# Optimization experiments

Hardware: AMD Instinct MI355X
Metric: run time of the kernel (lower is better)

## Reference

```python
import jax, jax.numpy as jnp
import numpy as np

D_MODEL = 1024
N_HEADS = 16
HEAD_DIM = D_MODEL // N_HEADS


def setup_inputs() -> dict:
    key = jax.random.key(0)
    ks = jax.random.split(key, 5)
    x = jax.random.normal(ks[0], (4, 2048, D_MODEL), dtype=jnp.float32)
    s = 1.0 / np.sqrt(D_MODEL)
    W_qkv = jax.random.normal(ks[1], (D_MODEL, 3 * D_MODEL), dtype=jnp.float32) * s
    b_qkv = jnp.zeros((3 * D_MODEL,), dtype=jnp.float32)
    W_proj = jax.random.normal(ks[2], (D_MODEL, D_MODEL), dtype=jnp.float32) * s
    b_proj = jnp.zeros((D_MODEL,), dtype=jnp.float32)
    return {"x": x, "W_qkv": W_qkv, "b_qkv": b_qkv, "W_proj": W_proj, "b_proj": b_proj}


def reference(x, W_qkv, b_qkv, W_proj, b_proj):
    B, T, C = x.shape
    H, Dh = N_HEADS, HEAD_DIM
    qkv = x @ W_qkv + b_qkv                      # [B,T,3C]
    q, k, v = jnp.split(qkv, 3, axis=-1)
    # [B,T,C] -> [B,H,T,Dh]
    q = q.reshape(B, T, H, Dh).transpose(0, 2, 1, 3)
    k = k.reshape(B, T, H, Dh).transpose(0, 2, 1, 3)
    v = v.reshape(B, T, H, Dh).transpose(0, 2, 1, 3)
    scale = 1.0 / np.sqrt(Dh)
    att = jnp.einsum("bhqd,bhkd->bhqk", q, k) * scale
    causal = jnp.tril(jnp.ones((T, T), dtype=bool))
    att = jnp.where(causal, att, -jnp.inf)
    att = jax.nn.softmax(att, axis=-1)
    y = jnp.einsum("bhqk,bhkd->bhqd", att, v)    # [B,H,T,Dh]
    y = y.transpose(0, 2, 1, 3).reshape(B, T, C)
    return y @ W_proj + b_proj
```

## Files before the change

### kernel.cpp

```cpp
#include <hip/hip_runtime.h>
#include <hip/hip_bf16.h>
#include <cstdint>
#include <math.h>

#define DM   1024
#define NH   16
#define DH   64
#define BB   4
#define TT   2048
#define MTOT (BB*TT)

using short8 = __attribute__((ext_vector_type(8))) short;
using f32x4  = __attribute__((ext_vector_type(4))) float;

__device__ __forceinline__ f32x4 mfma16(short8 a, short8 b, f32x4 c) {
  return __builtin_amdgcn_mfma_f32_16x16x32_bf16(a, b, c, 0, 0, 0);
}

typedef const __attribute__((address_space(1))) unsigned int* as1_u32p;
typedef __attribute__((address_space(3))) unsigned int*       as3_u32p;

__device__ __forceinline__ void gl_lds16(const void* g, void* l) {
  __builtin_amdgcn_global_load_lds(
      (as1_u32p)(reinterpret_cast<uintptr_t>(g)),
      (as3_u32p)((unsigned int)(reinterpret_cast<uintptr_t>(l))),
      16, 0, 0);
}

__device__ __forceinline__ int swz64(int row, int col) {
  return row*64 + ((((col >> 3) ^ (row & 7)) << 3) | (col & 7));
}

__device__ __forceinline__ unsigned pkbf(float a, float b) {
  __hip_bfloat162 h = __float22bfloat162_rn(make_float2(a, b));
  return *reinterpret_cast<unsigned*>(&h);
}

__device__ __forceinline__ void perm16p(unsigned &a, unsigned &b) {
  asm("v_permlane16_swap_b32 %0, %1" : "+v"(a), "+v"(b));
}
__device__ __forceinline__ void perm32p(unsigned &a, unsigned &b) {
  asm("v_permlane32_swap_b32 %0, %1" : "+v"(a), "+v"(b));
}

__device__ __forceinline__ short8 ldsr_o0(unsigned a) {
  short8 r; asm volatile("ds_read_b128 %0, %1" : "=v"(r) : "v"(a)); return r;
}
__device__ __forceinline__ short8 ldsr_o1(unsigned a) {
  short8 r; asm volatile("ds_read_b128 %0, %1 offset:2048" : "=v"(r) : "v"(a)); return r;
}
__device__ __forceinline__ short8 ldsr_o2(unsigned a) {
  short8 r; asm volatile("ds_read_b128 %0, %1 offset:4096" : "=v"(r) : "v"(a)); return r;
}
__device__ __forceinline__ short8 ldsr_o3(unsigned a) {
  short8 r; asm volatile("ds_read_b128 %0, %1 offset:6144" : "=v"(r) : "v"(a)); return r;
}

#define LGKM0  do { asm volatile("s_waitcnt lgkmcnt(0)"); __builtin_amdgcn_sched_barrier(0); } while(0)
#define VMCNT6 do { __builtin_amdgcn_sched_barrier(0); asm volatile("s_waitcnt vmcnt(6)"); __builtin_amdgcn_sched_barrier(0); } while(0)
#define VMCNT0 do { __builtin_amdgcn_sched_barrier(0); asm volatile("s_waitcnt vmcnt(0)"); __builtin_amdgcn_sched_barrier(0); } while(0)
#define BARRIER do { __builtin_amdgcn_s_barrier(); __builtin_amdgcn_sched_barrier(0); } while(0)

__global__ __launch_bounds__(256) void k_cvt(const float* __restrict__ in,
                                             __hip_bfloat16* __restrict__ out, int n8) {
  int i = blockIdx.x * 256 + threadIdx.x;
  if (i >= n8) return;
  const float* p = in + (size_t)i * 8;
  short8 o;
#pragma unroll
  for (int j = 0; j < 8; ++j) {
    __hip_bfloat16 h = __float2bfloat16(p[j]);
    o[j] = *reinterpret_cast<short*>(&h);
  }
  *reinterpret_cast<short8*>(out + (size_t)i * 8) = o;
}

__global__ __launch_bounds__(256) void k_transpose_cvt(const float* __restrict__ W,
                                                       __hip_bfloat16* __restrict__ Wt,
                                                       int K, int N) {
  __shared__ float tbuf[32][33];
  const int n0 = blockIdx.x * 32, k0 = blockIdx.y * 32;
  const int tx = threadIdx.x & 31, ty = threadIdx.x >> 5;
#pragma unroll
  for (int i = 0; i < 4; ++i)
    tbuf[ty + i*8][tx] = W[(size_t)(k0 + ty + i*8) * N + n0 + tx];
  __syncthreads();
#pragma unroll
  for (int i = 0; i < 4; ++i)
    Wt[(size_t)(n0 + ty + i*8) * K + k0 + tx] = __float2bfloat16(tbuf[tx][ty + i*8]);
}

template <int EPI>
__global__ __launch_bounds__(512, 2) void k_gemm2(const __hip_bfloat16* __restrict__ A,
                                                  const __hip_bfloat16* __restrict__ Bt,
                                                  const float* __restrict__ bias,
                                                  float* __restrict__ outF,
                                                  __hip_bfloat16* __restrict__ Qb,
                                                  __hip_bfloat16* __restrict__ Kb,
                                                  __hip_bfloat16* __restrict__ Vtb) {
  __shared__ __hip_bfloat16 As[3][256 * 64];
  __shared__ __hip_bfloat16 Bs[3][128 * 64];
  const int tid = threadIdx.x;
  const int l = tid & 63, w = tid >> 6;
  const int lr = l & 15, lg = l >> 4;
  const int wm = w >> 1, wn = w & 1;
  const int m0 = blockIdx.x * 256, n0 = blockIdx.y * 128;

  const int srow = tid >> 3;
  const int scol = (((tid & 7) ^ (srow & 7)) << 3);
  const size_t aoffs = (size_t)(m0 + srow) * 1024 + scol;
  const size_t boffs = (size_t)(n0 + srow) * 1024 + scol;
  const int ldst = tid * 8;

  auto stage = [&](int t, int s) {
    const int k0 = t * 64;
    __hip_bfloat16* as_ = &As[s][0];
    __hip_bfloat16* bs_ = &Bs[s][0];
#pragma unroll
    for (int rd = 0; rd < 4; ++rd)
      gl_lds16(A + aoffs + (size_t)rd * 65536 + k0, as_ + rd * 4096 + ldst);
#pragma unroll
    for (int rd = 0; rd < 2; ++rd)
      gl_lds16(Bt + boffs + (size_t)rd * 65536 + k0, bs_ + rd * 4096 + ldst);
  };

  const unsigned asLds = (unsigned)(uintptr_t)&As[0][0];
  const unsigned bsLds = (unsigned)(uintptr_t)&Bs[0][0];
  const unsigned aBase = asLds + 2u * ((wm*64 + lr) * 64 + ((lg ^ (lr & 7)) << 3));
  const unsigned bBase = bsLds + 2u * ((wn*64 + lr) * 64 + ((lg ^ (lr & 7)) << 3));

  stage(0, 0);
  stage(1, 1);
  VMCNT6;
  BARRIER;

  f32x4 acc[4][4] = {};
  short8 a_[4][2], b_[2][2];

#pragma unroll
  for (int t = 0; t < 16; ++t) {
    const int s = t % 3;
    const unsigned aB0 = aBase + (unsigned)s * 32768u;
    const unsigned aB1 = aB0 ^ 64u;
    const unsigned bB0 = bBase + (unsigned)s * 16384u;
    const unsigned bB1 = bB0 ^ 64u;
    if (t + 2 < 16) stage(t + 2, (t + 2) % 3);
    a_[0][0] = ldsr_o0(aB0); a_[1][0] = ldsr_o1(aB0); a_[2][0] = ldsr_o2(aB0); a_[3][0] = ldsr_o3(aB0);
    a_[0][1] = ldsr_o0(aB1); a_[1][1] = ldsr_o1(aB1); a_[2][1] = ldsr_o2(aB1); a_[3][1] = ldsr_o3(aB1);
    b_[0][0] = ldsr_o0(bB0); b_[1][0] = ldsr_o1(bB0);
    b_[0][1] = ldsr_o0(bB1); b_[1][1] = ldsr_o1(bB1);
    LGKM0;
    __builtin_amdgcn_s_setprio(1);
#pragma unroll
    for (int m = 0; m < 4; ++m)
#pragma unroll
      for (int n = 0; n < 2; ++n)
#pragma unroll
        for (int ks = 0; ks < 2; ++ks)
          acc[m][n] = mfma16(a_[m][ks], b_[n][ks], acc[m][n]);
    __builtin_amdgcn_s_setprio(0);
    b_[0][0] = ldsr_o2(bB0); b_[1][0] = ldsr_o3(bB0);
    b_[0][1] = ldsr_o2(bB1); b_[1][1] = ldsr_o3(bB1);
    LGKM0;
    __builtin_amdgcn_s_setprio(1);
#pragma unroll
    for (int m = 0; m < 4; ++m)
#pragma unroll
      for (int n = 0; n < 2; ++n)
#pragma unroll
        for (int ks = 0; ks < 2; ++ks)
          acc[m][n + 2] = mfma16(a_[m][ks], b_[n][ks], acc[m][n + 2]);
    __builtin_amdgcn_s_setprio(0);
    if (t <= 13) { VMCNT6; }
    else if (t == 14) { VMCNT0; }
    BARRIER;
  }

  __syncthreads();
  if (EPI == 0) {
    __hip_bfloat16* reg = &As[0][0] + w * 4096;
    const int colbase = n0 + wn * 64;
    const int which = colbase >> 10;
    const int hh = (colbase >> 6) & 15;
    const float qs = 0.18033688011112042f;
#pragma unroll
    for (int n = 0; n < 4; ++n) {
      const int lc = n * 16 + lr;
      const float bv = bias[colbase + lc];
#pragma unroll
      for (int m = 0; m < 4; ++m) {
#pragma unroll
        for (int r = 0; r < 4; ++r) {
          const int lrow = m * 16 + lg * 4 + r;
          float v = acc[m][n][r] + bv;
          if (which == 0) v *= qs;
          const __hip_bfloat16 hv = __float2bfloat16(v);
          if (which == 2) reg[swz64(lc, lrow)] = hv;
          else            reg[swz64(lrow, lc)] = hv;
        }
      }
    }
    const int rowbase = m0 + wm * 64;
    const int b = rowbase >> 11;
    const size_t bh = (size_t)b * 16 + hh;
    const int g = l >> 2, i = l & 3;
    if (which < 2) {
      __hip_bfloat16* base = (which == 0) ? Qb : Kb;
#pragma unroll
      for (int j = 0; j < 4; ++j) {
        const int lrow = j * 16 + g;
        const int t = (rowbase & 2047) + lrow;
        __hip_bfloat16* dst = base + (bh * TT + t) * 64 + i * 16;
        short8 y0 = *reinterpret_cast<const short8*>(&reg[swz64(lrow, i * 16)]);
        short8 y1 = *reinterpret_cast<const short8*>(&reg[swz64(lrow, i * 16 + 8)]);
        *reinterpret_cast<short8*>(dst) = y0;
        *reinterpret_cast<short8*>(dst + 8) = y1;
      }
    } else {
#pragma unroll
      for (int j = 0; j < 4; ++j) {
        const int dd = j * 16 + g;
        const int t = (rowbase & 2047) + i * 16;
        __hip_bfloat16* dst = Vtb + (bh * 64 + dd) * TT + t;
        short8 y0 = *reinterpret_cast<const short8*>(&reg[swz64(dd, i * 16)]);
        short8 y1 = *reinterpret_cast<const short8*>(&reg[swz64(dd, i * 16 + 8)]);
        *reinterpret_cast<short8*>(dst) = y0;
        *reinterpret_cast<short8*>(dst + 8) = y1;
      }
    }
  } else {
#pragma unroll
    for (int n = 0; n < 4; ++n) {
      const int col = n0 + wn * 64 + n * 16 + lr;
      const float bv = bias[col];
#pragma unroll
      for (int m = 0; m < 4; ++m)
#pragma unroll
        for (int r = 0; r < 4; ++r) {
          const int row = m0 + wm * 64 + m * 16 + lg * 4 + r;
          outF[(size_t)row * 1024 + col] = acc[m][n][r] + bv;
        }
    }
  }
}

__device__ __forceinline__ void tile_step(f32x4 s0, f32x4 s1, int kbase, int kmaxw, int qmb,
                                          short8 v0, short8 v1, short8 v2, short8 v3,
                                          f32x4 (&acc)[4], float& lrun) {
  if (kbase + 31 > kmaxw - 15) {
#pragma unroll
    for (int r = 0; r < 4; ++r) {
      const int off = (r & 1) + ((r & 2) << 2);
      if (kbase + off > qmb)      s0[r] = -INFINITY;
      if (kbase + 16 + off > qmb) s1[r] = -INFINITY;
    }
  }
  float p0 = __builtin_amdgcn_exp2f(s0[0]), p1 = __builtin_amdgcn_exp2f(s0[1]);
  float p2 = __builtin_amdgcn_exp2f(s0[2]), p3 = __builtin_amdgcn_exp2f(s0[3]);
  float p4 = __builtin_amdgcn_exp2f(s1[0]), p5 = __builtin_amdgcn_exp2f(s1[1]);
  float p6 = __builtin_amdgcn_exp2f(s1[2]), p7 = __builtin_amdgcn_exp2f(s1[3]);
  lrun += ((p0 + p1) + (p2 + p3)) + ((p4 + p5) + (p6 + p7));
  unsigned u0 = pkbf(p0, p1);
  unsigned u1 = pkbf(p2, p3);
  unsigned u2 = pkbf(p4, p5);
  unsigned u3 = pkbf(p6, p7);
  perm16p(u0, u1);
  perm16p(u2, u3);
  perm32p(u0, u2);
  perm32p(u1, u3);
  union { unsigned u[4]; short8 s; } pw;
  pw.u[0] = u0; pw.u[1] = u2; pw.u[2] = u1; pw.u[3] = u3;
  const short8 pf = pw.s;
  acc[0] = mfma16(v0, pf, acc[0]);
  acc[1] = mfma16(v1, pf, acc[1]);
  acc[2] = mfma16(v2, pf, acc[2]);
  acc[3] = mfma16(v3, pf, acc[3]);
}

__device__ __forceinline__ void store_tile(__hip_bfloat16* Ylds, f32x4 (&acc)[4],
                                           float lrun, int q0, int w, int l,
                                           int lr, int lg, int bh,
                                           __hip_bfloat16* __restrict__ Y) {
  lrun += __shfl_xor(lrun, 16);
  lrun += __shfl_xor(lrun, 32);
  const float inv = 1.f / lrun;
#pragma unroll
  for (int nb = 0; nb < 4; ++nb) {
#pragma unroll
    for (int r = 0; r < 4; ++r) {
      const int d = nb * 16 + lg * 4 + r;
      Ylds[swz64(lr, d)] = __float2bfloat16(acc[nb][r] * inv);
    }
  }
  const int rr = l >> 2, part = l & 3;
  const int trow = q0 + w * 16 + rr;
  const int b = bh >> 4, h = bh & 15;
  short8 y0 = *reinterpret_cast<const short8*>(&Ylds[swz64(rr, part * 16)]);
  short8 y1 = *reinterpret_cast<const short8*>(&Ylds[swz64(rr, part * 16 + 8)]);
  __hip_bfloat16* dst = Y + ((size_t)b * TT + trow) * 1024 + h * 64 + part * 16;
  *reinterpret_cast<short8*>(dst) = y0;
  *reinterpret_cast<short8*>(dst + 8) = y1;
}

__global__ __launch_bounds__(256, 4) void k_flash(const __hip_bfloat16* __restrict__ Qb,
                                                  const __hip_bfloat16* __restrict__ Kb,
                                                  const __hip_bfloat16* __restrict__ Vtb,
                                                  __hip_bfloat16* __restrict__ Y) {
  __shared__ __hip_bfloat16 Klds[128 * 64];
  __shared__ __hip_bfloat16 Vtlds[64 * 128];
  const int tid = threadIdx.x;
  const int l = tid & 63, w = tid >> 6;
  const int lr = l & 15, lg = l >> 4;
  const int p  = blockIdx.x >> 6;
  const int bh = blockIdx.x & 63;
  const int q0A = p * 64, q0B = (31 - p) * 64;
  const __hip_bfloat16* Qp = Qb + (size_t)bh * TT * 64;
  const __hip_bfloat16* Kp = Kb + (size_t)bh * TT * 64;
  const __hip_bfloat16* Vp = Vtb + (size_t)bh * 64 * TT;
  const int qrowA = q0A + w * 16 + lr;
  const int qrowB = q0B + w * 16 + lr;
  const short8 qfA0 = *reinterpret_cast<const short8*>(Qp + (size_t)qrowA * 64 + lg * 8);
  const short8 qfA1 = *reinterpret_cast<const short8*>(Qp + (size_t)qrowA * 64 + 32 + lg * 8);
  const short8 qfB0 = *reinterpret_cast<const short8*>(Qp + (size_t)qrowB * 64 + lg * 8);
  const short8 qfB1 = *reinterpret_cast<const short8*>(Qp + (size_t)qrowB * 64 + 32 + lg * 8);
  f32x4 accA[4] = {}, accB[4] = {};
  float lA = 0.f, lB = 0.f;

  const int ka  = lr * 64 + ((lg ^ (lr & 7)) << 3);
  const int va  = lr * 128 + ((lg ^ (lr & 15)) << 3);

  const __hip_bfloat16* gk[4];
  const __hip_bfloat16* gv[4];
  __hip_bfloat16* lk[4];
  __hip_bfloat16* lv[4];
#pragma unroll
  for (int it = 0; it < 4; ++it) {
    int e = it * 2048 + tid * 8;
    int rowk = e >> 6;
    int lcolk = ((((e >> 3) & 7) ^ (rowk & 7)) << 3);
    int rk = rowk & 15;
    int srk = (((rk >> 1) ^ (rk >> 3)) & 1) ? (rk ^ 10) : rk;
    int rowks = (rowk & ~15) | srk;
    gk[it] = Kp + (size_t)rowks * 64 + lcolk;
    lk[it] = &Klds[e];
    int rowv = e >> 7;
    int lcolv = ((((e >> 3) & 15) ^ (rowv & 15)) << 3);
    gv[it] = Vp + (size_t)rowv * TT + lcolv;
    lv[it] = &Vtlds[e];
  }

  const int kmaxwA = q0A + w * 16 + 15;
  const int kmaxwB = q0B + w * 16 + 15;
  const int base_lg = ((lg & 1) << 2) | (lg & 2);
  const int qmbA = qrowA - base_lg;
  const int qmbB = qrowB - base_lg;
  const int nblk = (q0B + 63) / 128 + 1;
  for (int blk = 0; blk < nblk; ++blk) {
    const int kv0 = blk * 128;
#pragma unroll
    for (int it = 0; it < 4; ++it) {
      gl_lds16(gk[it], lk[it]);
      gk[it] += 128 * 64;
    }
#pragma unroll
    for (int it = 0; it < 4; ++it) {
      gl_lds16(gv[it], lv[it]);
      gv[it] += 128;
    }
    __syncthreads();
#pragma unroll
    for (int kci = 0; kci < 4; ++kci) {
      const int kbase = kv0 + kci * 32;
      if (kbase > kmaxwB) break;
      const int kb = ka + kci * 2048;
      const short8 kf00 = *reinterpret_cast<const short8*>(&Klds[kb]);
      const short8 kf10 = *reinterpret_cast<const short8*>(&Klds[kb + 1024]);
      const short8 kf01 = *reinterpret_cast<const short8*>(&Klds[kb ^ 32]);
      const short8 kf11 = *reinterpret_cast<const short8*>(&Klds[(kb + 1024) ^ 32]);
      f32x4 sB0 = {}, sB1 = {};
      sB0 = mfma16(kf00, qfB0, sB0);
      sB1 = mfma16(kf10, qfB0, sB1);
      sB0 = mfma16(kf01, qfB1, sB0);
      sB1 = mfma16(kf11, qfB1, sB1);
      const bool aAct = (kbase <= kmaxwA);
      f32x4 sA0 = {}, sA1 = {};
      if (aAct) {
        sA0 = mfma16(kf00, qfA0, sA0);
        sA1 = mfma16(kf10, qfA0, sA1);
        sA0 = mfma16(kf01, qfA1, sA0);
        sA1 = mfma16(kf11, qfA1, sA1);
      }
      const int vb = va ^ (kci * 32);
      const short8 v0 = *reinterpret_cast<const short8*>(&Vtlds[vb]);
      const short8 v1 = *reinterpret_cast<const short8*>(&Vtlds[vb + 2048]);
      const short8 v2 = *reinterpret_cast<const short8*>(&Vtlds[vb + 4096]);
      const short8 v3 = *reinterpret_cast<const short8*>(&Vtlds[vb + 6144]);
      tile_step(sB0, sB1, kbase, kmaxwB, qmbB, v0, v1, v2, v3, accB, lB);
      if (aAct)
        tile_step(sA0, sA1, kbase, kmaxwA, qmbA, v0, v1, v2, v3, accA, lA);
    }
    __syncthreads();
  }
  __hip_bfloat16* Ylds = Klds + w * 1024;
  store_tile(Ylds, accA, lA, q0A, w, l, lr, lg, bh, Y);
  store_tile(Ylds, accB, lB, q0B, w, l, lr, lg, bh, Y);
}

extern "C" void kernel_launch(void* const* d_in, const int* in_sizes, int n_in,
                              void* d_out, int out_size, void* d_ws, size_t ws_size,
                              hipStream_t stream) {
  const float* x     = (const float*)d_in[0];
  const float* Wqkv  = (const float*)d_in[1];
  const float* bqkv  = (const float*)d_in[2];
  const float* Wproj = (const float*)d_in[3];
  const float* bproj = (const float*)d_in[4];

  char* ws = (char*)d_ws;
  size_t off = 0;
  auto alloc = [&](size_t bytes) {
    char* p = ws + off;
    off += (bytes + 255) & ~(size_t)255;
    return p;
  };
  __hip_bfloat16* xb    = (__hip_bfloat16*)alloc((size_t)MTOT * 1024 * 2);
  __hip_bfloat16* wqkvT = (__hip_bfloat16*)alloc((size_t)3072 * 1024 * 2);
  __hip_bfloat16* wpT   = (__hip_bfloat16*)alloc((size_t)1024 * 1024 * 2);
  __hip_bfloat16* Qb    = (__hip_bfloat16*)alloc((size_t)64 * TT * 64 * 2);
  __hip_bfloat16* Kb    = (__hip_bfloat16*)alloc((size_t)64 * TT * 64 * 2);
  __hip_bfloat16* Vtb   = (__hip_bfloat16*)alloc((size_t)64 * TT * 64 * 2);
  __hip_bfloat16* Yb    = (__hip_bfloat16*)alloc((size_t)MTOT * 1024 * 2);

  k_cvt<<<(MTOT * 1024 / 8 + 255) / 256, 256, 0, stream>>>(x, xb, MTOT * 1024 / 8);
  k_transpose_cvt<<<dim3(3072 / 32, 1024 / 32), 256, 0, stream>>>(Wqkv, wqkvT, 1024, 3072);
  k_transpose_cvt<<<dim3(1024 / 32, 1024 / 32), 256, 0, stream>>>(Wproj, wpT, 1024, 1024);
  k_gemm2<0><<<dim3(32, 24), 512, 0, stream>>>(xb, wqkvT, bqkv, nullptr, Qb, Kb, Vtb);
  k_flash<<<16 * 64, 256, 0, stream>>>(Qb, Kb, Vtb, Yb);
  k_gemm2<1><<<dim3(32, 8), 512, 0, stream>>>(Yb, wpT, bproj, (float*)d_out,
                                              nullptr, nullptr, nullptr);
}
```

Baseline: 152.3 us.

## Add dedicated QKV GEMM kernel with 256x192 tiles and double buffering

Adds a separate QKV projection kernel that uses 256x192 output tiles instead of 256x128, with a 2-stage LDS pipeline in place of 3 stages. Each wave accumulates a 64x96 sub-tile in two MFMA phases. The grid drops from 32x24 to 32x16 blocks, so each block reuses its A tile across more columns. The epilogue is rewritten to scatter Q/K/V per 16-column group through LDS. The risks are higher register pressure from 24 accumulators per wave, shallower prefetch with a full vmcnt(0) wait every iteration, and possible tail effects from the new block count.

```diff
diff --git a/kernel.cpp b/kernel.cpp
--- a/kernel.cpp
+++ b/kernel.cpp
@@ -55,6 +55,12 @@
 __device__ __forceinline__ short8 ldsr_o3(unsigned a) {
   short8 r; asm volatile("ds_read_b128 %0, %1 offset:6144" : "=v"(r) : "v"(a)); return r;
 }
+__device__ __forceinline__ short8 ldsr_o4(unsigned a) {
+  short8 r; asm volatile("ds_read_b128 %0, %1 offset:8192" : "=v"(r) : "v"(a)); return r;
+}
+__device__ __forceinline__ short8 ldsr_o5(unsigned a) {
+  short8 r; asm volatile("ds_read_b128 %0, %1 offset:10240" : "=v"(r) : "v"(a)); return r;
+}
 
 #define LGKM0  do { asm volatile("s_waitcnt lgkmcnt(0)"); __builtin_amdgcn_sched_barrier(0); } while(0)
 #define VMCNT6 do { __builtin_amdgcn_sched_barrier(0); asm volatile("s_waitcnt vmcnt(6)"); __builtin_amdgcn_sched_barrier(0); } while(0)
@@ -90,14 +96,156 @@
     Wt[(size_t)(n0 + ty + i*8) * K + k0 + tx] = __float2bfloat16(tbuf[tx][ty + i*8]);
 }
 
-template <int EPI>
+__global__ __launch_bounds__(512, 2) void k_gemm3(const __hip_bfloat16* __restrict__ A,
+                                                  const __hip_bfloat16* __restrict__ Bt,
+                                                  const float* __restrict__ bias,
+                                                  __hip_bfloat16* __restrict__ Qb,
+                                                  __hip_bfloat16* __restrict__ Kb,
+                                                  __hip_bfloat16* __restrict__ Vtb) {
+  __shared__ __hip_bfloat16 As[2][256 * 64];
+  __shared__ __hip_bfloat16 Bs[2][192 * 64];
+  const int tid = threadIdx.x;
+  const int l = tid & 63, w = tid >> 6;
+  const int lr = l & 15, lg = l >> 4;
+  const int wm = w >> 1, wn = w & 1;
+  const int m0 = blockIdx.x * 256, n0 = blockIdx.y * 192;
+
+  const int srow = tid >> 3;
+  const int scol = (((tid & 7) ^ (srow & 7)) << 3);
+  const size_t aoffs = (size_t)(m0 + srow) * 1024 + scol;
+  const size_t boffs = (size_t)(n0 + srow) * 1024 + scol;
+  const int ldst = tid * 8;
+
+  auto stage = [&](int t, int s) {
+    const int k0 = t * 64;
+#pragma unroll
+    for (int rd = 0; rd < 4; ++rd)
+      gl_lds16(A + aoffs + (size_t)rd * 65536 + k0, &As[s][rd * 4096 + ldst]);
+#pragma unroll
+    for (int rd = 0; rd < 3; ++rd)
+      gl_lds16(Bt + boffs + (size_t)rd * 65536 + k0, &Bs[s][rd * 4096 + ldst]);
+  };
+
+  const unsigned asLds = (unsigned)(uintptr_t)&As[0][0];
+  const unsigned bsLds = (unsigned)(uintptr_t)&Bs[0][0];
+  const unsigned aBase0 = asLds + 2u * ((wm*64 + lr) * 64 + ((lg ^ (lr & 7)) << 3));
+  const unsigned bBase0 = bsLds + 2u * ((wn*96 + lr) * 64 + ((lg ^ (lr & 7)) << 3));
+
+  stage(0, 0);
+  VMCNT0;
+  BARRIER;
+
+  f32x4 acc[4][6] = {};
+  short8 a_[4][2], b_[3][2];
+
+#pragma unroll
+  for (int t = 0; t < 16; ++t) {
+    const int s = t & 1;
+    const unsigned aB0 = aBase0 + (unsigned)s * 32768u;
+    const unsigned aB1 = aB0 ^ 64u;
+    const unsigned bB0 = bBase0 + (unsigned)s * 24576u;
+    const unsigned bB1 = bB0 ^ 64u;
+    if (t < 15) stage(t + 1, s ^ 1);
+    a_[0][0] = ldsr_o0(aB0); a_[1][0] = ldsr_o1(aB0); a_[2][0] = ldsr_o2(aB0); a_[3][0] = ldsr_o3(aB0);
+    a_[0][1] = ldsr_o0(aB1); a_[1][1] = ldsr_o1(aB1); a_[2][1] = ldsr_o2(aB1); a_[3][1] = ldsr_o3(aB1);
+    b_[0][0] = ldsr_o0(bB0); b_[1][0] = ldsr_o1(bB0); b_[2][0] = ldsr_o2(bB0);
+    b_[0][1] = ldsr_o0(bB1); b_[1][1] = ldsr_o1(bB1); b_[2][1] = ldsr_o2(bB1);
+    LGKM0;
+    __builtin_amdgcn_s_setprio(1);
+#pragma unroll
+    for (int m = 0; m < 4; ++m)
+#pragma unroll
+      for (int n = 0; n < 3; ++n)
+#pragma unroll
+        for (int ks = 0; ks < 2; ++ks)
+          acc[m][n] = mfma16(a_[m][ks], b_[n][ks], acc[m][n]);
+    __builtin_amdgcn_s_setprio(0);
+    b_[0][0] = ldsr_o3(bB0); b_[1][0] = ldsr_o4(bB0); b_[2][0] = ldsr_o5(bB0);
+    b_[0][1] = ldsr_o3(bB1); b_[1][1] = ldsr_o4(bB1); b_[2][1] = ldsr_o5(bB1);
+    LGKM0;
+    __builtin_amdgcn_s_setprio(1);
+#pragma unroll
+    for (int m = 0; m < 4; ++m)
+#pragma unroll
+      for (int n = 0; n < 3; ++n)
+#pragma unroll
+        for (int ks = 0; ks < 2; ++ks)
+          acc[m][n + 3] = mfma16(a_[m][ks], b_[n][ks], acc[m][n + 3]);
+    __builtin_amdgcn_s_setprio(0);
+    if (t < 15) { VMCNT0; }
+    BARRIER;
+  }
+
+  __syncthreads();
+  __hip_bfloat16* reg = (w < 4) ? (&As[0][0] + w * 6144)
+                                : (&Bs[0][0] + (w - 4) * 6144);
+  const int colbase = n0 + wn * 96;
+  const int rowbase = m0 + wm * 64;
+  const int bidx = rowbase >> 11;
+  const int tbase = rowbase & 2047;
+  const float qs = 0.18033688011112042f;
+  float bv[6];
+#pragma unroll
+  for (int g = 0; g < 6; ++g) bv[g] = bias[colbase + g * 16 + lr];
+#pragma unroll
+  for (int g = 0; g < 6; ++g) {
+    const int cg0 = colbase + g * 16;
+    const int which = cg0 >> 10;
+    __hip_bfloat16* rg = reg + g * 1024;
+    if (which == 2) {
+#pragma unroll
+      for (int m = 0; m < 4; ++m)
+#pragma unroll
+        for (int r = 0; r < 4; ++r) {
+          const int t = m * 16 + lg * 4 + r;
+          rg[lr * 64 + (t ^ ((lr & 7) << 3))] = __float2bfloat16(acc[m][g][r] + bv[g]);
+        }
+    } else {
+      const float sc = (which == 0) ? qs : 1.f;
+#pragma unroll
+      for (int m = 0; m < 4; ++m)
+#pragma unroll
+        for (int r = 0; r < 4; ++r) {
+          const int t = m * 16 + lg * 4 + r;
+          rg[t * 16 + (lr ^ (((t >> 2) & 1) << 3))] =
+              __float2bfloat16((acc[m][g][r] + bv[g]) * sc);
+        }
+    }
+  }
+#pragma unroll
+  for (int g = 0; g < 6; ++g) {
+    const int cg0 = colbase + g * 16;
+    const int which = cg0 >> 10;
+    const int hh = (cg0 >> 6) & 15;
+    const int dd0 = cg0 & 48;
+    const size_t bh = (size_t)bidx * 16 + hh;
+    const __hip_bfloat16* rg = reg + g * 1024;
+    if (which < 2) {
+      __hip_bfloat16* basep = (which == 0) ? Qb : Kb;
+      const int t = l;
+      const int Xc = ((t >> 2) & 1) << 3;
+      short8 y0 = *reinterpret_cast<const short8*>(&rg[t * 16 + Xc]);
+      short8 y1 = *reinterpret_cast<const short8*>(&rg[t * 16 + (Xc ^ 8)]);
+      __hip_bfloat16* dst = basep + (bh * TT + tbase + t) * 64 + dd0;
+      *reinterpret_cast<short8*>(dst) = y0;
+      *reinterpret_cast<short8*>(dst + 8) = y1;
+    } else {
+      const int dd = l >> 2, tseg = l & 3;
+      const int X = (dd & 7) << 3;
+      const int S0 = (((tseg ^ (X >> 4)) & 3) << 4) | (X & 8);
+      short8 y0 = *reinterpret_cast<const short8*>(&rg[dd * 64 + S0]);
+      short8 y1 = *reinterpret_cast<const short8*>(&rg[dd * 64 + (S0 ^ 8)]);
+      __hip_bfloat16* dst = Vtb + (bh * 64 + dd0 + dd) * TT + tbase + tseg * 16;
+      *reinterpret_cast<short8*>(dst) = y0;
+      *reinterpret_cast<short8*>(dst + 8) = y1;
+    }
+  }
+}
+
 __global__ __launch_bounds__(512, 2) void k_gemm2(const __hip_bfloat16* __restrict__ A,
                                                   const __hip_bfloat16* __restrict__ Bt,
                                                   const float* __restrict__ bias,
-                                                  float* __restrict__ outF,
-                                                  __hip_bfloat16* __restrict__ Qb,
-                                                  __hip_bfloat16* __restrict__ Kb,
-                                                  __hip_bfloat16* __restrict__ Vtb) {
+                                                  float* __restrict__ outF) {
   __shared__ __hip_bfloat16 As[3][256 * 64];
   __shared__ __hip_bfloat16 Bs[3][128 * 64];
   const int tid = threadIdx.x;
@@ -177,70 +325,17 @@
   }
 
   __syncthreads();
-  if (EPI == 0) {
-    __hip_bfloat16* reg = &As[0][0] + w * 4096;
-    const int colbase = n0 + wn * 64;
-    const int which = colbase >> 10;
-    const int hh = (colbase >> 6) & 15;
-    const float qs = 0.18033688011112042f;
-#pragma unroll
-    for (int n = 0; n < 4; ++n) {
-      const int lc = n * 16 + lr;
-      const float bv = bias[colbase + lc];
-#pragma unroll
-      for (int m = 0; m < 4; ++m) {
-#pragma unroll
-        for (int r = 0; r < 4; ++r) {
-          const int lrow = m * 16 + lg * 4 + r;
-          float v = acc[m][n][r] + bv;
-          if (which == 0) v *= qs;
-          const __hip_bfloat16 hv = __float2bfloat16(v);
-          if (which == 2) reg[swz64(lc, lrow)] = hv;
-          else            reg[swz64(lrow, lc)] = hv;
-        }
+#pragma unroll
+  for (int n = 0; n < 4; ++n) {
+    const int col = n0 + wn * 64 + n * 16 + lr;
+    const float bvv = bias[col];
+#pragma unroll
+    for (int m = 0; m < 4; ++m)
+#pragma unroll
+      for (int r = 0; r < 4; ++r) {
+        const int row = m0 + wm * 64 + m * 16 + lg * 4 + r;
+        outF[(size_t)row * 1024 + col] = acc[m][n][r] + bvv;
       }
-    }
-    const int rowbase = m0 + wm * 64;
-    const int b = rowbase >> 11;
-    const size_t bh = (size_t)b * 16 + hh;
-    const int g = l >> 2, i = l & 3;
-    if (which < 2) {
-      __hip_bfloat16* base = (which == 0) ? Qb : Kb;
-#pragma unroll
-      for (int j = 0; j < 4; ++j) {
-        const int lrow = j * 16 + g;
-        const int t = (rowbase & 2047) + lrow;
-        __hip_bfloat16* dst = base + (bh * TT + t) * 64 + i * 16;
-        short8 y0 = *reinterpret_cast<const short8*>(&reg[swz64(lrow, i * 16)]);
-        short8 y1 = *reinterpret_cast<const short8*>(&reg[swz64(lrow, i * 16 + 8)]);
-        *reinterpret_cast<short8*>(dst) = y0;
-        *reinterpret_cast<short8*>(dst + 8) = y1;
-      }
-    } else {
-#pragma unroll
-      for (int j = 0; j < 4; ++j) {
-        const int dd = j * 16 + g;
-        const int t = (rowbase & 2047) + i * 16;
-        __hip_bfloat16* dst = Vtb + (bh * 64 + dd) * TT + t;
-        short8 y0 = *reinterpret_cast<const short8*>(&reg[swz64(dd, i * 16)]);
-        short8 y1 = *reinterpret_cast<const short8*>(&reg[swz64(dd, i * 16 + 8)]);
-        *reinterpret_cast<short8*>(dst) = y0;
-        *reinterpret_cast<short8*>(dst + 8) = y1;
-      }
-    }
-  } else {
-#pragma unroll
-    for (int n = 0; n < 4; ++n) {
-      const int col = n0 + wn * 64 + n * 16 + lr;
-      const float bv = bias[col];
-#pragma unroll
-      for (int m = 0; m < 4; ++m)
-#pragma unroll
-        for (int r = 0; r < 4; ++r) {
-          const int row = m0 + wm * 64 + m * 16 + lg * 4 + r;
-          outF[(size_t)row * 1024 + col] = acc[m][n][r] + bv;
-        }
-    }
   }
 }
 
@@ -433,8 +528,7 @@
   k_cvt<<<(MTOT * 1024 / 8 + 255) / 256, 256, 0, stream>>>(x, xb, MTOT * 1024 / 8);
   k_transpose_cvt<<<dim3(3072 / 32, 1024 / 32), 256, 0, stream>>>(Wqkv, wqkvT, 1024, 3072);
   k_transpose_cvt<<<dim3(1024 / 32, 1024 / 32), 256, 0, stream>>>(Wproj, wpT, 1024, 1024);
-  k_gemm2<0><<<dim3(32, 24), 512, 0, stream>>>(xb, wqkvT, bqkv, nullptr, Qb, Kb, Vtb);
+  k_gemm3<<<dim3(32, 16), 512, 0, stream>>>(xb, wqkvT, bqkv, Qb, Kb, Vtb);
   k_flash<<<16 * 64, 256, 0, stream>>>(Qb, Kb, Vtb, Yb);
-  k_gemm2<1><<<dim3(32, 8), 512, 0, stream>>>(Yb, wpT, bproj, (float*)d_out,
-                                              nullptr, nullptr, nullptr);
-}
+  k_gemm2<<<dim3(32, 8), 512, 0, stream>>>(Yb, wpT, bproj, (float*)d_out);
+}
```

New measurement: 147.1 us. 3.4% less time.

## Use 256x256 tiled QKV GEMM with 4-stage K=32 pipeline

Applied to the files above, without the earlier changes.

The QKV projection gets its own kernel with a 256x256 output tile per block (8 waves as 2x4) instead of 256x128. Each stage now covers K=32, with a new row-pair swizzled LDS layout and four stages in flight. The larger tile raises arithmetic intensity per LDS byte and halves the grid to 384 blocks. In exchange it uses more accumulator registers (128 floats per lane), which may hurt occupancy or spill, and the smaller grid fills the CUs less evenly. The output projection keeps the old 256x128 kernel, now without the template parameter.

```diff
diff --git a/kernel.cpp b/kernel.cpp
--- a/kernel.cpp
+++ b/kernel.cpp
@@ -43,21 +43,35 @@
   asm("v_permlane32_swap_b32 %0, %1" : "+v"(a), "+v"(b));
 }
 
-__device__ __forceinline__ short8 ldsr_o0(unsigned a) {
+__device__ __forceinline__ short8 ldsr_p0(unsigned a) {
   short8 r; asm volatile("ds_read_b128 %0, %1" : "=v"(r) : "v"(a)); return r;
 }
-__device__ __forceinline__ short8 ldsr_o1(unsigned a) {
+__device__ __forceinline__ short8 ldsr_p1(unsigned a) {
+  short8 r; asm volatile("ds_read_b128 %0, %1 offset:1024" : "=v"(r) : "v"(a)); return r;
+}
+__device__ __forceinline__ short8 ldsr_p2(unsigned a) {
   short8 r; asm volatile("ds_read_b128 %0, %1 offset:2048" : "=v"(r) : "v"(a)); return r;
 }
-__device__ __forceinline__ short8 ldsr_o2(unsigned a) {
+__device__ __forceinline__ short8 ldsr_p3(unsigned a) {
+  short8 r; asm volatile("ds_read_b128 %0, %1 offset:3072" : "=v"(r) : "v"(a)); return r;
+}
+__device__ __forceinline__ short8 ldsr_p4(unsigned a) {
   short8 r; asm volatile("ds_read_b128 %0, %1 offset:4096" : "=v"(r) : "v"(a)); return r;
 }
-__device__ __forceinline__ short8 ldsr_o3(unsigned a) {
+__device__ __forceinline__ short8 ldsr_p5(unsigned a) {
+  short8 r; asm volatile("ds_read_b128 %0, %1 offset:5120" : "=v"(r) : "v"(a)); return r;
+}
+__device__ __forceinline__ short8 ldsr_p6(unsigned a) {
   short8 r; asm volatile("ds_read_b128 %0, %1 offset:6144" : "=v"(r) : "v"(a)); return r;
 }
+__device__ __forceinline__ short8 ldsr_p7(unsigned a) {
+  short8 r; asm volatile("ds_read_b128 %0, %1 offset:7168" : "=v"(r) : "v"(a)); return r;
+}
 
 #define LGKM0  do { asm volatile("s_waitcnt lgkmcnt(0)"); __builtin_amdgcn_sched_barrier(0); } while(0)
+#define VMCNT8 do { __builtin_amdgcn_sched_barrier(0); asm volatile("s_waitcnt vmcnt(8)"); __builtin_amdgcn_sched_barrier(0); } while(0)
 #define VMCNT6 do { __builtin_amdgcn_sched_barrier(0); asm volatile("s_waitcnt vmcnt(6)"); __builtin_amdgcn_sched_barrier(0); } while(0)
+#define VMCNT4 do { __builtin_amdgcn_sched_barrier(0); asm volatile("s_waitcnt vmcnt(4)"); __builtin_amdgcn_sched_barrier(0); } while(0)
 #define VMCNT0 do { __builtin_amdgcn_sched_barrier(0); asm volatile("s_waitcnt vmcnt(0)"); __builtin_amdgcn_sched_barrier(0); } while(0)
 #define BARRIER do { __builtin_amdgcn_s_barrier(); __builtin_amdgcn_sched_barrier(0); } while(0)
 
@@ -90,99 +104,85 @@
     Wt[(size_t)(n0 + ty + i*8) * K + k0 + tx] = __float2bfloat16(tbuf[tx][ty + i*8]);
 }
 
-template <int EPI>
-__global__ __launch_bounds__(512, 2) void k_gemm2(const __hip_bfloat16* __restrict__ A,
+__global__ __launch_bounds__(512, 2) void k_gemm3(const __hip_bfloat16* __restrict__ A,
                                                   const __hip_bfloat16* __restrict__ Bt,
                                                   const float* __restrict__ bias,
-                                                  float* __restrict__ outF,
                                                   __hip_bfloat16* __restrict__ Qb,
                                                   __hip_bfloat16* __restrict__ Kb,
                                                   __hip_bfloat16* __restrict__ Vtb) {
-  __shared__ __hip_bfloat16 As[3][256 * 64];
-  __shared__ __hip_bfloat16 Bs[3][128 * 64];
+  __shared__ __hip_bfloat16 Ls[4][16384];
   const int tid = threadIdx.x;
   const int l = tid & 63, w = tid >> 6;
   const int lr = l & 15, lg = l >> 4;
-  const int wm = w >> 1, wn = w & 1;
-  const int m0 = blockIdx.x * 256, n0 = blockIdx.y * 128;
-
-  const int srow = tid >> 3;
-  const int scol = (((tid & 7) ^ (srow & 7)) << 3);
-  const size_t aoffs = (size_t)(m0 + srow) * 1024 + scol;
-  const size_t boffs = (size_t)(n0 + srow) * 1024 + scol;
-  const int ldst = tid * 8;
+  const int lr2 = lr >> 1;
+  const int wm = w >> 2, wn = w & 3;
+  const int m0 = blockIdx.x * 256, n0 = blockIdx.y * 256;
+
+  size_t aoffs[2], boffs[2];
+#pragma unroll
+  for (int j = 0; j < 2; ++j) {
+    const int e = j * 4096 + tid * 8;
+    const int rr = e >> 6;
+    const int c8 = ((e >> 3) & 7) ^ (rr & 7);
+    const int rg = rr * 2 + (c8 >> 2);
+    const int ko = (c8 & 3) * 8;
+    aoffs[j] = (size_t)(m0 + rg) * 1024 + ko;
+    boffs[j] = (size_t)(n0 + rg) * 1024 + ko;
+  }
+  const int ld0 = tid * 8;
 
   auto stage = [&](int t, int s) {
-    const int k0 = t * 64;
-    __hip_bfloat16* as_ = &As[s][0];
-    __hip_bfloat16* bs_ = &Bs[s][0];
-#pragma unroll
-    for (int rd = 0; rd < 4; ++rd)
-      gl_lds16(A + aoffs + (size_t)rd * 65536 + k0, as_ + rd * 4096 + ldst);
-#pragma unroll
-    for (int rd = 0; rd < 2; ++rd)
-      gl_lds16(Bt + boffs + (size_t)rd * 65536 + k0, bs_ + rd * 4096 + ldst);
+    const int kb = t * 32;
+    __hip_bfloat16* base = &Ls[s][0];
+    gl_lds16(A + aoffs[0] + kb, base + ld0);
+    gl_lds16(A + aoffs[1] + kb, base + 4096 + ld0);
+    gl_lds16(Bt + boffs[0] + kb, base + 8192 + ld0);
+    gl_lds16(Bt + boffs[1] + kb, base + 12288 + ld0);
   };
 
-  const unsigned asLds = (unsigned)(uintptr_t)&As[0][0];
-  const unsigned bsLds = (unsigned)(uintptr_t)&Bs[0][0];
-  const unsigned aBase = asLds + 2u * ((wm*64 + lr) * 64 + ((lg ^ (lr & 7)) << 3));
-  const unsigned bBase = bsLds + 2u * ((wn*64 + lr) * 64 + ((lg ^ (lr & 7)) << 3));
-
-  stage(0, 0);
-  stage(1, 1);
-  VMCNT6;
+  const unsigned asLds = (unsigned)(uintptr_t)&Ls[0][0];
+  const unsigned fslot = (unsigned)((((lr & 1) << 2) | lg) ^ (lr2 & 7));
+  const unsigned laneA = (unsigned)(lr2 * 128) + fslot * 16u;
+  const unsigned aLane = asLds + (unsigned)(wm * 8192) + laneA;
+  const unsigned bLane = asLds + 16384u + (unsigned)(wn * 4096) + laneA;
+
+  stage(0, 0); stage(1, 1); stage(2, 2);
+  VMCNT8;
   BARRIER;
 
-  f32x4 acc[4][4] = {};
-  short8 a_[4][2], b_[2][2];
-
-#pragma unroll
-  for (int t = 0; t < 16; ++t) {
-    const int s = t % 3;
-    const unsigned aB0 = aBase + (unsigned)s * 32768u;
-    const unsigned aB1 = aB0 ^ 64u;
-    const unsigned bB0 = bBase + (unsigned)s * 16384u;
-    const unsigned bB1 = bB0 ^ 64u;
-    if (t + 2 < 16) stage(t + 2, (t + 2) % 3);
-    a_[0][0] = ldsr_o0(aB0); a_[1][0] = ldsr_o1(aB0); a_[2][0] = ldsr_o2(aB0); a_[3][0] = ldsr_o3(aB0);
-    a_[0][1] = ldsr_o0(aB1); a_[1][1] = ldsr_o1(aB1); a_[2][1] = ldsr_o2(aB1); a_[3][1] = ldsr_o3(aB1);
-    b_[0][0] = ldsr_o0(bB0); b_[1][0] = ldsr_o1(bB0);
-    b_[0][1] = ldsr_o0(bB1); b_[1][1] = ldsr_o1(bB1);
+  f32x4 acc[8][4] = {};
+  short8 a_[8], b_[4];
+
+#pragma unroll 4
+  for (int t = 0; t < 32; ++t) {
+    const int s = t & 3;
+    const unsigned aB = aLane + (unsigned)s * 32768u;
+    const unsigned bB = bLane + (unsigned)s * 32768u;
+    if (t < 29) stage(t + 3, (t + 3) & 3);
+    a_[0] = ldsr_p0(aB); a_[1] = ldsr_p1(aB); a_[2] = ldsr_p2(aB); a_[3] = ldsr_p3(aB);
+    a_[4] = ldsr_p4(aB); a_[5] = ldsr_p5(aB); a_[6] = ldsr_p6(aB); a_[7] = ldsr_p7(aB);
+    b_[0] = ldsr_p0(bB); b_[1] = ldsr_p1(bB); b_[2] = ldsr_p2(bB); b_[3] = ldsr_p3(bB);
     LGKM0;
     __builtin_amdgcn_s_setprio(1);
 #pragma unroll
-    for (int m = 0; m < 4; ++m)
-#pragma unroll
-      for (int n = 0; n < 2; ++n)
-#pragma unroll
-        for (int ks = 0; ks < 2; ++ks)
-          acc[m][n] = mfma16(a_[m][ks], b_[n][ks], acc[m][n]);
+    for (int ni = 0; ni < 4; ++ni)
+#pragma unroll
+      for (int mi = 0; mi < 8; ++mi)
+        acc[mi][ni] = mfma16(a_[mi], b_[ni], acc[mi][ni]);
     __builtin_amdgcn_s_setprio(0);
-    b_[0][0] = ldsr_o2(bB0); b_[1][0] = ldsr_o3(bB0);
-    b_[0][1] = ldsr_o2(bB1); b_[1][1] = ldsr_o3(bB1);
-    LGKM0;
-    __builtin_amdgcn_s_setprio(1);
-#pragma unroll
-    for (int m = 0; m < 4; ++m)
-#pragma unroll
-      for (int n = 0; n < 2; ++n)
-#pragma unroll
-        for (int ks = 0; ks < 2; ++ks)
-          acc[m][n + 2] = mfma16(a_[m][ks], b_[n][ks], acc[m][n + 2]);
-    __builtin_amdgcn_s_setprio(0);
-    if (t <= 13) { VMCNT6; }
-    else if (t == 14) { VMCNT0; }
-    BARRIER;
+    if (t <= 28)      { VMCNT8; BARRIER; }
+    else if (t == 29) { VMCNT4; BARRIER; }
+    else if (t == 30) { VMCNT0; BARRIER; }
   }
 
   __syncthreads();
-  if (EPI == 0) {
-    __hip_bfloat16* reg = &As[0][0] + w * 4096;
-    const int colbase = n0 + wn * 64;
-    const int which = colbase >> 10;
-    const int hh = (colbase >> 6) & 15;
-    const float qs = 0.18033688011112042f;
+  __hip_bfloat16* reg = &Ls[0][0] + w * 4096;
+  const int colbase = n0 + wn * 64;
+  const int which = colbase >> 10;
+  const int hh = (colbase >> 6) & 15;
+  const float qs = 0.18033688011112042f;
+#pragma unroll
+  for (int h = 0; h < 2; ++h) {
 #pragma unroll
     for (int n = 0; n < 4; ++n) {
       const int lc = n * 16 + lr;
@@ -192,7 +192,7 @@
 #pragma unroll
         for (int r = 0; r < 4; ++r) {
           const int lrow = m * 16 + lg * 4 + r;
-          float v = acc[m][n][r] + bv;
+          float v = acc[h * 4 + m][n][r] + bv;
           if (which == 0) v *= qs;
           const __hip_bfloat16 hv = __float2bfloat16(v);
           if (which == 2) reg[swz64(lc, lrow)] = hv;
@@ -200,17 +200,17 @@
         }
       }
     }
-    const int rowbase = m0 + wm * 64;
+    const int rowbase = m0 + wm * 128 + h * 64;
     const int b = rowbase >> 11;
     const size_t bh = (size_t)b * 16 + hh;
     const int g = l >> 2, i = l & 3;
     if (which < 2) {
-      __hip_bfloat16* base = (which == 0) ? Qb : Kb;
+      __hip_bfloat16* basep = (which == 0) ? Qb : Kb;
 #pragma unroll
       for (int j = 0; j < 4; ++j) {
         const int lrow = j * 16 + g;
         const int t = (rowbase & 2047) + lrow;
-        __hip_bfloat16* dst = base + (bh * TT + t) * 64 + i * 16;
+        __hip_bfloat16* dst = basep + (bh * TT + t) * 64 + i * 16;
         short8 y0 = *reinterpret_cast<const short8*>(&reg[swz64(lrow, i * 16)]);
         short8 y1 = *reinterpret_cast<const short8*>(&reg[swz64(lrow, i * 16 + 8)]);
         *reinterpret_cast<short8*>(dst) = y0;
@@ -228,19 +228,104 @@
         *reinterpret_cast<short8*>(dst + 8) = y1;
       }
     }
-  } else {
-#pragma unroll
-    for (int n = 0; n < 4; ++n) {
-      const int col = n0 + wn * 64 + n * 16 + lr;
-      const float bv = bias[col];
-#pragma unroll
-      for (int m = 0; m < 4; ++m)
-#pragma unroll
-        for (int r = 0; r < 4; ++r) {
-          const int row = m0 + wm * 64 + m * 16 + lg * 4 + r;
-          outF[(size_t)row * 1024 + col] = acc[m][n][r] + bv;
-        }
-    }
+  }
+}
+
+__device__ __forceinline__ short8 ldsr_o0(unsigned a) { return ldsr_p0(a); }
+__global__ __launch_bounds__(512, 2) void k_gemm2(const __hip_bfloat16* __restrict__ A,
+                                                  const __hip_bfloat16* __restrict__ Bt,
+                                                  const float* __restrict__ bias,
+                                                  float* __restrict__ outF) {
+  __shared__ __hip_bfloat16 As[3][256 * 64];
+  __shared__ __hip_bfloat16 Bs[3][128 * 64];
+  const int tid = threadIdx.x;
+  const int l = tid & 63, w = tid >> 6;
+  const int lr = l & 15, lg = l >> 4;
+  const int wm = w >> 1, wn = w & 1;
+  const int m0 = blockIdx.x * 256, n0 = blockIdx.y * 128;
+
+  const int srow = tid >> 3;
+  const int scol = (((tid & 7) ^ (srow & 7)) << 3);
+  const size_t aoffs = (size_t)(m0 + srow) * 1024 + scol;
+  const size_t boffs = (size_t)(n0 + srow) * 1024 + scol;
+  const int ldst = tid * 8;
+
+  auto stage = [&](int t, int s) {
+    const int k0 = t * 64;
+    __hip_bfloat16* as_ = &As[s][0];
+    __hip_bfloat16* bs_ = &Bs[s][0];
+#pragma unroll
+    for (int rd = 0; rd < 4; ++rd)
+      gl_lds16(A + aoffs + (size_t)rd * 65536 + k0, as_ + rd * 4096 + ldst);
+#pragma unroll
+    for (int rd = 0; rd < 2; ++rd)
+      gl_lds16(Bt + boffs + (size_t)rd * 65536 + k0, bs_ + rd * 4096 + ldst);
+  };
+
+  const unsigned asLds = (unsigned)(uintptr_t)&As[0][0];
+  const unsigned bsLds = (unsigned)(uintptr_t)&Bs[0][0];
+  const unsigned aBase = asLds + 2u * ((wm*64 + lr) * 64 + ((lg ^ (lr & 7)) << 3));
+  const unsigned bBase = bsLds + 2u * ((wn*64 + lr) * 64 + ((lg ^ (lr & 7)) << 3));
+
+  stage(0, 0);
+  stage(1, 1);
+  VMCNT6;
+  BARRIER;
+
+  f32x4 acc[4][4] = {};
+  short8 a_[4][2], b_[2][2];
+
+#pragma unroll
+  for (int t = 0; t < 16; ++t) {
+    const int s = t % 3;
+    const unsigned aB0 = aBase + (unsigned)s * 32768u;
+    const unsigned aB1 = aB0 ^ 64u;
+    const unsigned bB0 = bBase + (unsigned)s * 16384u;
+    const unsigned bB1 = bB0 ^ 64u;
+    if (t + 2 < 16) stage(t + 2, (t + 2) % 3);
+    a_[0][0] = ldsr_p0(aB0); a_[1][0] = ldsr_p2(aB0); a_[2][0] = ldsr_p4(aB0); a_[3][0] = ldsr_p6(aB0);
+    a_[0][1] = ldsr_p0(aB1); a_[1][1] = ldsr_p2(aB1); a_[2][1] = ldsr_p4(aB1); a_[3][1] = ldsr_p6(aB1);
+    b_[0][0] = ldsr_p0(bB0); b_[1][0] = ldsr_p2(bB0);
+    b_[0][1] = ldsr_p0(bB1); b_[1][1] = ldsr_p2(bB1);
+    LGKM0;
+    __builtin_amdgcn_s_setprio(1);
+#pragma unroll
+    for (int m = 0; m < 4; ++m)
+#pragma unroll
+      for (int n = 0; n < 2; ++n)
+#pragma unroll
+        for (int ks = 0; ks < 2; ++ks)
+          acc[m][n] = mfma16(a_[m][ks], b_[n][ks], acc[m][n]);
+    __builtin_amdgcn_s_setprio(0);
+    b_[0][0] = ldsr_p4(bB0); b_[1][0] = ldsr_p6(bB0);
+    b_[0][1] = ldsr_p4(bB1); b_[1][1] = ldsr_p6(bB1);
+    LGKM0;
+    __builtin_amdgcn_s_setprio(1);
+#pragma unroll
+    for (int m = 0; m < 4; ++m)
+#pragma unroll
+      for (int n = 0; n < 2; ++n)
+#pragma unroll
+        for (int ks = 0; ks < 2; ++ks)
+          acc[m][n + 2] = mfma16(a_[m][ks], b_[n][ks], acc[m][n + 2]);
+    __builtin_amdgcn_s_setprio(0);
+    if (t <= 13) { VMCNT6; }
+    else if (t == 14) { VMCNT0; }
+    BARRIER;
+  }
+
+  __syncthreads();
+#pragma unroll
+  for (int n = 0; n < 4; ++n) {
+    const int col = n0 + wn * 64 + n * 16 + lr;
+    const float bvv = bias[col];
+#pragma unroll
+    for (int m = 0; m < 4; ++m)
+#pragma unroll
+      for (int r = 0; r < 4; ++r) {
+        const int row = m0 + wm * 64 + m * 16 + lg * 4 + r;
+        outF[(size_t)row * 1024 + col] = acc[m][n][r] + bvv;
+      }
   }
 }
 
@@ -433,8 +518,7 @@
   k_cvt<<<(MTOT * 1024 / 8 + 255) / 256, 256, 0, stream>>>(x, xb, MTOT * 1024 / 8);
   k_transpose_cvt<<<dim3(3072 / 32, 1024 / 32), 256, 0, stream>>>(Wqkv, wqkvT, 1024, 3072);
   k_transpose_cvt<<<dim3(1024 / 32, 1024 / 32), 256, 0, stream>>>(Wproj, wpT, 1024, 1024);
-  k_gemm2<0><<<dim3(32, 24), 512, 0, stream>>>(xb, wqkvT, bqkv, nullptr, Qb, Kb, Vtb);
+  k_gemm3<<<dim3(32, 12), 512, 0, stream>>>(xb, wqkvT, bqkv, Qb, Kb, Vtb);
   k_flash<<<16 * 64, 256, 0, stream>>>(Qb, Kb, Vtb, Yb);
-  k_gemm2<1><<<dim3(32, 8), 512, 0, stream>>>(Yb, wpT, bproj, (float*)d_out,
-                                              nullptr, nullptr, nullptr);
-}
+  k_gemm2<<<dim3(32, 8), 512, 0, stream>>>(Yb, wpT, bproj, (float*)d_out);
+}
```

After: 189.5 us. 24.4% more time.
